# Kernel tuning notes

Measured on AMD Instinct MI355X. Metric: run time of the kernel, lower is better.

## Reference

```python
import jax, jax.numpy as jnp
import numpy as np

V, BS, L, H, D, DF = 32000, 2048, 4, 4, 256, 1024
B, T = 2, 2048
DH = D // H


def setup_inputs() -> dict:
    key = jax.random.key(0)
    ks = iter(jax.random.split(key, 32))
    s = 0.02
    rn = lambda shape: jax.random.normal(next(ks), shape, jnp.float32) * s
    inp = {
        'idx': jax.random.randint(next(ks), (B, T), 0, V),
        'tok_emb': rn((V, D)),
        'pos_emb': rn((BS, D)),
        'Wq': rn((L, D, D)), 'bq': jnp.zeros((L, D)),
        'Wk': rn((L, D, D)), 'bk': jnp.zeros((L, D)),
        'Wv': rn((L, D, D)), 'bv': jnp.zeros((L, D)),
        'Wo': rn((L, D, D)), 'bo': jnp.zeros((L, D)),
        'ln1_g': jnp.ones((L, D)), 'ln1_b': jnp.zeros((L, D)),
        'W1': rn((L, D, DF)), 'b1': jnp.zeros((L, DF)),
        'W2': rn((L, DF, D)), 'b2': jnp.zeros((L, D)),
        'ln2_g': jnp.ones((L, D)), 'ln2_b': jnp.zeros((L, D)),
        'lnf_g': jnp.ones((D,)), 'lnf_b': jnp.zeros((D,)),
        'head_W': rn((D, V)), 'head_b': jnp.zeros((V,)),
    }
    return inp


def _layernorm(x, g, b, eps=1e-5):
    mu = jnp.mean(x, axis=-1, keepdims=True)
    var = jnp.mean(jnp.square(x - mu), axis=-1, keepdims=True)
    return (x - mu) * jax.lax.rsqrt(var + eps) * g + b


def reference(idx, tok_emb, pos_emb, Wq, bq, Wk, bk, Wv, bv, Wo, bo,
              ln1_g, ln1_b, W1, b1, W2, b2, ln2_g, ln2_b,
              lnf_g, lnf_b, head_W, head_b):
    b, t = idx.shape
    x = tok_emb[idx] + pos_emb[:t]  # [B,T,D]
    causal = jnp.tril(jnp.ones((t, t), dtype=bool))  # [T,T]
    scale = 1.0 / np.sqrt(DH)
    neg_inf = jnp.finfo(x.dtype).min
    for l in range(L):
        h = _layernorm(x, ln1_g[l], ln1_b[l])
        q = (h @ Wq[l] + bq[l]).reshape(b, t, H, DH)
        k = (h @ Wk[l] + bk[l]).reshape(b, t, H, DH)
        v = (h @ Wv[l] + bv[l]).reshape(b, t, H, DH)
        att = jnp.einsum('bqhd,bkhd->bhqk', q, k) * scale
        att = jnp.where(causal, att, neg_inf)
        att = jax.nn.softmax(att, axis=-1)
        y = jnp.einsum('bhqk,bkhd->bqhd', att, v).reshape(b, t, D)
        x = x + (y @ Wo[l] + bo[l])
        h = _layernorm(x, ln2_g[l], ln2_b[l])
        x = x + (jax.nn.gelu(h @ W1[l] + b1[l], approximate=False) @ W2[l] + b2[l])
    x = _layernorm(x, lnf_g, lnf_b)
    return x @ head_W + head_b  # [B,T,V]
```

## Files before the change

### kernel.cpp

```cpp
#include <hip/hip_runtime.h>
#include <hip/hip_bf16.h>
#include <math.h>

#define V_   32000
#define L_   4
#define H_   4
#define D_   256
#define DF_  1024
#define B_   2
#define T_   2048
#define DH_  64
#define NTOK (B_*T_)

typedef __attribute__((ext_vector_type(8))) short bf16x8;
typedef __attribute__((ext_vector_type(4))) float f32x4;
typedef unsigned short u16;

#define GLOAD16(gsrc, ldst) \
  __builtin_amdgcn_global_load_lds((const __attribute__((address_space(1))) void*)(gsrc), \
                                   (__attribute__((address_space(3))) void*)(ldst), 16, 0, 0)

#define BAR_A()   asm volatile("s_barrier" ::: "memory")
#define WAITB(N)  do { asm volatile("s_waitcnt vmcnt(" #N ") lgkmcnt(0)" ::: "memory"); \
                       asm volatile("s_barrier" ::: "memory"); } while (0)

__device__ __forceinline__ u16 f2bf(float f) {
    unsigned int u = __builtin_bit_cast(unsigned int, f);
    u = (u + 0x7fff + ((u >> 16) & 1)) >> 16;
    return (u16)u;
}

__device__ __forceinline__ int xcd_swizzle(int orig, int nwg) {
    return ((nwg & 7) == 0) ? ((orig & 7) * (nwg >> 3) + (orig >> 3)) : orig;
}

__global__ __launch_bounds__(256) void prep_kernel(
    const float* __restrict__ Wq, const float* __restrict__ Wk,
    const float* __restrict__ Wv, const float* __restrict__ Wo,
    const float* __restrict__ W1, const float* __restrict__ W2,
    const float* __restrict__ hW,
    u16* __restrict__ WqkvT, u16* __restrict__ WoT,
    u16* __restrict__ W1T, u16* __restrict__ W2T, u16* __restrict__ hWT)
{
    int b = blockIdx.x;
    const float* src; u16* dst; int K, N, k0, n0;
    if (b < 512) {
        int m = b >> 5, t = b & 31;
        int wt = m & 3, l = m >> 2;
        K = 256; N = 256;
        src = (wt == 0 ? Wq : wt == 1 ? Wk : wt == 2 ? Wv : Wo) + (size_t)l * 65536;
        dst = (wt < 3) ? WqkvT + (size_t)l * 196608 + (size_t)wt * 65536
                       : WoT + (size_t)l * 65536;
        k0 = (t >> 3) * 64; n0 = (t & 7) * 32;
    } else if (b < 1024) {
        int bb = b - 512; int l = bb >> 7, t = bb & 127;
        K = 256; N = 1024;
        src = W1 + (size_t)l * 262144; dst = W1T + (size_t)l * 262144;
        k0 = (t >> 5) * 64; n0 = (t & 31) * 32;
    } else if (b < 1536) {
        int bb = b - 1024; int l = bb >> 7, t = bb & 127;
        K = 1024; N = 256;
        src = W2 + (size_t)l * 262144; dst = W2T + (size_t)l * 262144;
        k0 = (t >> 3) * 64; n0 = (t & 7) * 32;
    } else {
        int bb = b - 1536;
        K = 256; N = 32000;
        src = hW; dst = hWT;
        k0 = (bb / 1000) * 64; n0 = (bb % 1000) * 32;
    }
    __shared__ float tile[64][33];
    int tid = threadIdx.x;
    int tc = tid & 31, tr = tid >> 5;
    #pragma unroll
    for (int i = 0; i < 8; i++)
        tile[tr + i*8][tc] = src[(size_t)(k0 + tr + i*8) * N + n0 + tc];
    __syncthreads();
    int kc = tid & 63, nr = tid >> 6;
    #pragma unroll
    for (int i = 0; i < 8; i++)
        dst[(size_t)(n0 + nr + i*4) * K + k0 + kc] = f2bf(tile[kc][nr + i*4]);
}

__global__ __launch_bounds__(256) void embed_qkv_kernel(
    const int* __restrict__ idx, const float* __restrict__ tok, const float* __restrict__ pos,
    const float* __restrict__ g, const float* __restrict__ bta,
    const u16* __restrict__ WqkvT0,
    const float* __restrict__ bq, const float* __restrict__ bk, const float* __restrict__ bv,
    float* __restrict__ x, u16* __restrict__ qkv)
{
    __shared__ u16 Bs[2][256*64];
    __shared__ u16 hS[16][264];

    int tid = threadIdx.x;
    int lane = tid & 63, w = tid >> 6;
    int lr = lane & 15, lg = lane >> 4;
    int bid = xcd_swizzle(blockIdx.x, 256);
    int row0 = bid * 16;

    {
        int grow = tid >> 4;
        int gcol = (tid & 15) * 16;
        int n = row0 + grow;
        int t = n & (T_ - 1);
        int id = idx[n];
        float vv[16];
        #pragma unroll
        for (int i = 0; i < 4; i++) {
            float4 a = *(const float4*)(tok + (size_t)id * D_ + gcol + i * 4);
            float4 b = *(const float4*)(pos + (size_t)t * D_ + gcol + i * 4);
            vv[i*4+0] = a.x + b.x; vv[i*4+1] = a.y + b.y;
            vv[i*4+2] = a.z + b.z; vv[i*4+3] = a.w + b.w;
        }
        float s = 0.f, q = 0.f;
        #pragma unroll
        for (int i = 0; i < 16; i++) { s += vv[i]; q += vv[i]*vv[i]; }
        #pragma unroll
        for (int o = 1; o <= 8; o <<= 1) { s += __shfl_xor(s, o); q += __shfl_xor(q, o); }
        float mu = s * (1.0f / D_);
        float var = q * (1.0f / D_) - mu * mu;
        float ri = rsqrtf(var + 1e-5f);
        #pragma unroll
        for (int i = 0; i < 16; i++) {
            x[(size_t)n * D_ + gcol + i] = vv[i];
            hS[grow][gcol + i] = f2bf((vv[i] - mu) * ri * g[gcol + i] + bta[gcol + i]);
        }
    }

    auto stageQ = [&](int buf, int u) {
        const u16* BT = WqkvT0 + (size_t)(u >> 2) * 65536;
        int k0 = (u & 3) * 64;
        #pragma unroll
        for (int i = 0; i < 8; i++) {
            int o16 = tid + i * 256;
            int r = o16 >> 3;
            int sw = ((o16 & 7) << 4) ^ ((r & 7) << 4);
            GLOAD16(BT + (size_t)r * 256 + k0 + (sw >> 1), &Bs[buf][o16 * 8]);
        }
    };
    auto afH = [&](int t, int ks) -> bf16x8 {
        return *(const bf16x8*)(&hS[lr][(t * 128 + ks * 64 + lg * 16) >> 1]);
    };
    auto bfr = [&](int buf, int ni, int ks) -> bf16x8 {
        int rr = w * 64 + ni * 16 + lr;
        return *(const bf16x8*)(&Bs[buf][rr * 64 + (((ks * 64 + lg * 16) ^ ((rr & 7) << 4)) >> 1)]);
    };

    stageQ(0, 0);
    f32x4 acc[4] = {};
    for (int u = 0; u < 12; u++) {
        BAR_A();
        if (u + 1 < 12) { stageQ((u + 1) & 1, u + 1); WAITB(8); }
        else            { WAITB(0); }
        int t = u & 3;
        #pragma unroll
        for (int ks = 0; ks < 2; ks++) {
            bf16x8 a = afH(t, ks);
            __builtin_amdgcn_s_setprio(1);
            #pragma unroll
            for (int ni = 0; ni < 4; ni++)
                acc[ni] = __builtin_amdgcn_mfma_f32_16x16x32_bf16(a, bfr(u & 1, ni, ks), acc[ni], 0, 0, 0);
            __builtin_amdgcn_s_setprio(0);
        }
        if (t == 3) {
            int sel = u >> 2;
            const float* bp = sel == 0 ? bq : sel == 1 ? bk : bv;
            #pragma unroll
            for (int ni = 0; ni < 4; ni++) {
                #pragma unroll
                for (int j = 0; j < 4; j++) {
                    int row = row0 + lg * 4 + j;
                    int cc = w * 64 + ni * 16 + lr;
                    float v = acc[ni][j] + bp[cc];
                    int bb = row >> 11, tt = row & (T_ - 1);
                    int hh = cc >> 6, dh = cc & 63;
                    qkv[(size_t)sel * NTOK * D_ +
                        ((((size_t)bb * H_ + hh) * T_) + tt) * DH_ + dh] = f2bf(v);
                }
                acc[ni] = (f32x4){0.f, 0.f, 0.f, 0.f};
            }
        }
    }
}

__global__ __launch_bounds__(256) void wo_ln_kernel(
    const u16* __restrict__ ybuf, const u16* __restrict__ WoT, const float* __restrict__ bo,
    const float* __restrict__ ln2g, const float* __restrict__ ln2b,
    float* __restrict__ x, u16* __restrict__ hbuf)
{
    __shared__ u16 As[2][16*64];
    __shared__ u16 Bs[2][256*64];
    __shared__ float sred[4][16], qred[4][16];

    int tid = threadIdx.x;
    int lane = tid & 63, w = tid >> 6;
    int lr = lane & 15, lg = lane >> 4;
    int bid = xcd_swizzle(blockIdx.x, 256);
    int row0 = bid * 16;

    auto stage = [&](int buf, int k0) {
        #pragma unroll
        for (int i = 0; i < 8; i++) {
            int o16 = tid + i * 256;
            int r = o16 >> 3;
            int sw = ((o16 & 7) << 4) ^ ((r & 7) << 4);
            GLOAD16(WoT + (size_t)r * 256 + k0 + (sw >> 1), &Bs[buf][o16 * 8]);
        }
        if (tid < 128) {
            int r = tid >> 3;
            int sw = ((tid & 7) << 4) ^ ((r & 7) << 4);
            GLOAD16(ybuf + (size_t)(row0 + r) * 256 + k0 + (sw >> 1), &As[buf][tid * 8]);
        }
    };
    auto afA = [&](int buf, int ks) -> bf16x8 {
        return *(const bf16x8*)(&As[buf][lr * 64 + (((ks * 64 + lg * 16) ^ ((lr & 7) << 4)) >> 1)]);
    };
    auto bfr = [&](int buf, int ni, int ks) -> bf16x8 {
        int rr = w * 64 + ni * 16 + lr;
        return *(const bf16x8*)(&Bs[buf][rr * 64 + (((ks * 64 + lg * 16) ^ ((rr & 7) << 4)) >> 1)]);
    };

    stage(0, 0);
    f32x4 acc[4] = {};
    for (int t = 0; t < 4; t++) {
        BAR_A();
        if (t + 1 < 4) { stage((t + 1) & 1, (t + 1) * 64); WAITB(8); }
        else           { WAITB(0); }
        #pragma unroll
        for (int ks = 0; ks < 2; ks++) {
            bf16x8 a = afA(t & 1, ks);
            __builtin_amdgcn_s_setprio(1);
            #pragma unroll
            for (int ni = 0; ni < 4; ni++)
                acc[ni] = __builtin_amdgcn_mfma_f32_16x16x32_bf16(a, bfr(t & 1, ni, ks), acc[ni], 0, 0, 0);
            __builtin_amdgcn_s_setprio(0);
        }
    }

    float vals[4][4];
    float rs[4] = {0,0,0,0}, rq[4] = {0,0,0,0};
    #pragma unroll
    for (int ni = 0; ni < 4; ni++)
        #pragma unroll
        for (int j = 0; j < 4; j++) {
            int row = row0 + lg * 4 + j;
            int col = w * 64 + ni * 16 + lr;
            float v = acc[ni][j] + bo[col] + x[(size_t)row * D_ + col];
            x[(size_t)row * D_ + col] = v;
            vals[ni][j] = v;
            rs[j] += v; rq[j] += v * v;
        }
    #pragma unroll
    for (int j = 0; j < 4; j++)
        #pragma unroll
        for (int o = 1; o <= 8; o <<= 1) { rs[j] += __shfl_xor(rs[j], o); rq[j] += __shfl_xor(rq[j], o); }
    if (lr == 0)
        #pragma unroll
        for (int j = 0; j < 4; j++) { sred[w][lg*4 + j] = rs[j]; qred[w][lg*4 + j] = rq[j]; }
    __syncthreads();
    #pragma unroll
    for (int j = 0; j < 4; j++) {
        int r = lg * 4 + j;
        float mu = (sred[0][r] + sred[1][r] + sred[2][r] + sred[3][r]) * (1.0f / D_);
        float var = (qred[0][r] + qred[1][r] + qred[2][r] + qred[3][r]) * (1.0f / D_) - mu * mu;
        float ri = rsqrtf(var + 1e-5f);
        int row = row0 + r;
        #pragma unroll
        for (int ni = 0; ni < 4; ni++) {
            int col = w * 64 + ni * 16 + lr;
            hbuf[(size_t)row * D_ + col] = f2bf((vals[ni][j] - mu) * ri * ln2g[col] + ln2b[col]);
        }
    }
}

__global__ __launch_bounds__(256) void ff1_kernel(
    const u16* __restrict__ A, const u16* __restrict__ BT,
    const float* __restrict__ bias, u16* __restrict__ C)
{
    __shared__ u16 As[2][64*64];
    __shared__ u16 Bs[2][64*64];
    int tid = threadIdx.x;
    int lane = tid & 63, w = tid >> 6;
    int lr = lane & 15, lg = lane >> 4;
    int wm = w >> 1, wn = w & 1;

    int gx = gridDim.x;
    int nwg = gx * gridDim.y;
    int orig = blockIdx.y * gx + blockIdx.x;
    int bid = xcd_swizzle(orig, nwg);
    int row0 = (bid / gx) * 64, col0 = (bid % gx) * 64;

    auto stage = [&](int buf, int k0) {
        #pragma unroll
        for (int i = 0; i < 2; i++) {
            int o16 = tid + i * 256;
            int r = o16 >> 3;
            int sw = ((o16 & 7) << 4) ^ ((r & 7) << 4);
            GLOAD16(A + (size_t)(row0 + r) * 256 + k0 + (sw >> 1), &As[buf][o16 * 8]);
            GLOAD16(BT + (size_t)(col0 + r) * 256 + k0 + (sw >> 1), &Bs[buf][o16 * 8]);
        }
    };

    stage(0, 0);
    f32x4 acc[2][2] = {};
    for (int t = 0; t < 4; t++) {
        BAR_A();
        if (t + 1 < 4) { stage((t + 1) & 1, (t + 1) * 64); WAITB(4); }
        else           { WAITB(0); }
        #pragma unroll
        for (int ks = 0; ks < 2; ks++) {
            bf16x8 af[2], bfv[2];
            #pragma unroll
            for (int mi = 0; mi < 2; mi++) {
                int rr = wm * 32 + mi * 16 + lr;
                af[mi] = *(const bf16x8*)(&As[t & 1][rr * 64 + (((ks * 64 + lg * 16) ^ ((rr & 7) << 4)) >> 1)]);
            }
            #pragma unroll
            for (int ni = 0; ni < 2; ni++) {
                int rr = wn * 32 + ni * 16 + lr;
                bfv[ni] = *(const bf16x8*)(&Bs[t & 1][rr * 64 + (((ks * 64 + lg * 16) ^ ((rr & 7) << 4)) >> 1)]);
            }
            __builtin_amdgcn_s_setprio(1);
            #pragma unroll
            for (int mi = 0; mi < 2; mi++)
                #pragma unroll
                for (int ni = 0; ni < 2; ni++)
                    acc[mi][ni] = __builtin_amdgcn_mfma_f32_16x16x32_bf16(af[mi], bfv[ni], acc[mi][ni], 0, 0, 0);
            __builtin_amdgcn_s_setprio(0);
        }
    }

    #pragma unroll
    for (int mi = 0; mi < 2; mi++)
        #pragma unroll
        for (int ni = 0; ni < 2; ni++)
            #pragma unroll
            for (int j = 0; j < 4; j++) {
                int row = row0 + wm * 32 + mi * 16 + lg * 4 + j;
                int col = col0 + wn * 32 + ni * 16 + lr;
                float v = acc[mi][ni][j] + bias[col];
                v = 0.5f * v * (1.0f + erff(v * 0.70710678118f));
                C[(size_t)row * DF_ + col] = f2bf(v);
            }
}

template<bool LAST>
__global__ __launch_bounds__(256) void ff2qkv_kernel(
    const u16* __restrict__ ff, const u16* __restrict__ W2T, const float* __restrict__ b2,
    const float* __restrict__ lng, const float* __restrict__ lnb,
    const u16* __restrict__ WqkvT,
    const float* __restrict__ bq, const float* __restrict__ bk, const float* __restrict__ bv,
    float* __restrict__ x, u16* __restrict__ hout, u16* __restrict__ qkv)
{
    __shared__ u16 As[2][16*64];
    __shared__ u16 Bs[2][256*64];
    __shared__ u16 hS[16][264];
    __shared__ float sred[4][16], qred[4][16];

    int tid = threadIdx.x;
    int lane = tid & 63, w = tid >> 6;
    int lr = lane & 15, lg = lane >> 4;
    int bid = xcd_swizzle(blockIdx.x, 256);
    int row0 = bid * 16;

    auto stageB = [&](int buf, const u16* BT, int K, int k0) {
        #pragma unroll
        for (int i = 0; i < 8; i++) {
            int o16 = tid + i * 256;
            int r = o16 >> 3;
            int sw = ((o16 & 7) << 4) ^ ((r & 7) << 4);
            GLOAD16(BT + (size_t)r * K + k0 + (sw >> 1), &Bs[buf][o16 * 8]);
        }
    };
    auto stageA = [&](int buf, int k0) {
        if (tid < 128) {
            int r = tid >> 3;
            int sw = ((tid & 7) << 4) ^ ((r & 7) << 4);
            GLOAD16(ff + (size_t)(row0 + r) * DF_ + k0 + (sw >> 1), &As[buf][tid * 8]);
        }
    };
    auto prefetch = [&](int u) {
        if (u < 16) { stageA(u & 1, u * 64); stageB(u & 1, W2T, 1024, u * 64); }
        else if (!LAST && u < 28) {
            int v = u - 16;
            stageB(u & 1, WqkvT + (size_t)(v >> 2) * 65536, 256, (v & 3) * 64);
        }
    };
    auto afA = [&](int buf, int ks) -> bf16x8 {
        return *(const bf16x8*)(&As[buf][lr * 64 + (((ks * 64 + lg * 16) ^ ((lr & 7) << 4)) >> 1)]);
    };
    auto afH = [&](int t, int ks) -> bf16x8 {
        return *(const bf16x8*)(&hS[lr][(t * 128 + ks * 64 + lg * 16) >> 1]);
    };
    auto bfr = [&](int buf, int ni, int ks) -> bf16x8 {
        int rr = w * 64 + ni * 16 + lr;
        return *(const bf16x8*)(&Bs[buf][rr * 64 + (((ks * 64 + lg * 16) ^ ((rr & 7) << 4)) >> 1)]);
    };

    prefetch(0);
    f32x4 acc[4] = {};
    for (int u = 0; u < 16; u++) {
        BAR_A();
        prefetch(u + 1);
        WAITB(8);
        #pragma unroll
        for (int ks = 0; ks < 2; ks++) {
            bf16x8 a = afA(u & 1, ks);
            __builtin_amdgcn_s_setprio(1);
            #pragma unroll
            for (int ni = 0; ni < 4; ni++)
                acc[ni] = __builtin_amdgcn_mfma_f32_16x16x32_bf16(a, bfr(u & 1, ni, ks), acc[ni], 0, 0, 0);
            __builtin_amdgcn_s_setprio(0);
        }
    }

    {
        float vals[4][4];
        float rs[4] = {0,0,0,0}, rq[4] = {0,0,0,0};
        #pragma unroll
        for (int ni = 0; ni < 4; ni++)
            #pragma unroll
            for (int j = 0; j < 4; j++) {
                int row = row0 + lg * 4 + j;
                int col = w * 64 + ni * 16 + lr;
                float v = acc[ni][j] + b2[col] + x[(size_t)row * D_ + col];
                x[(size_t)row * D_ + col] = v;
                vals[ni][j] = v;
                rs[j] += v; rq[j] += v * v;
            }
        #pragma unroll
        for (int j = 0; j < 4; j++)
            #pragma unroll
            for (int o = 1; o <= 8; o <<= 1) { rs[j] += __shfl_xor(rs[j], o); rq[j] += __shfl_xor(rq[j], o); }
        if (lr == 0)
            #pragma unroll
            for (int j = 0; j < 4; j++) { sred[w][lg*4 + j] = rs[j]; qred[w][lg*4 + j] = rq[j]; }
        __syncthreads();
        #pragma unroll
        for (int j = 0; j < 4; j++) {
            int r = lg * 4 + j;
            float mu = (sred[0][r] + sred[1][r] + sred[2][r] + sred[3][r]) * (1.0f / D_);
            float var = (qred[0][r] + qred[1][r] + qred[2][r] + qred[3][r]) * (1.0f / D_) - mu * mu;
            float ri = rsqrtf(var + 1e-5f);
            #pragma unroll
            for (int ni = 0; ni < 4; ni++) {
                int col = w * 64 + ni * 16 + lr;
                float hv = (vals[ni][j] - mu) * ri * lng[col] + lnb[col];
                if (LAST) hout[(size_t)(row0 + r) * D_ + col] = f2bf(hv);
                else      hS[r][col] = f2bf(hv);
            }
        }
    }

    if constexpr (!LAST) {
        __syncthreads();
        f32x4 accT[4] = {};
        for (int v = 0; v < 12; v++) {
            BAR_A();
            if (v + 1 < 12) { prefetch(16 + v + 1); WAITB(8); }
            else            { WAITB(0); }
            int t = v & 3;
            #pragma unroll
            for (int ks = 0; ks < 2; ks++) {
                bf16x8 a = afH(t, ks);
                __builtin_amdgcn_s_setprio(1);
                #pragma unroll
                for (int ni = 0; ni < 4; ni++)
                    accT[ni] = __builtin_amdgcn_mfma_f32_16x16x32_bf16(a, bfr(v & 1, ni, ks), accT[ni], 0, 0, 0);
                __builtin_amdgcn_s_setprio(0);
            }
            if (t == 3) {
                int sel = v >> 2;
                const float* bp = sel == 0 ? bq : sel == 1 ? bk : bv;
                #pragma unroll
                for (int ni = 0; ni < 4; ni++) {
                    #pragma unroll
                    for (int j = 0; j < 4; j++) {
                        int row = row0 + lg * 4 + j;
                        int cc = w * 64 + ni * 16 + lr;
                        float val = accT[ni][j] + bp[cc];
                        int bb = row >> 11, tt = row & (T_ - 1);
                        int hh = cc >> 6, dh = cc & 63;
                        qkv[(size_t)sel * NTOK * D_ +
                            ((((size_t)bb * H_ + hh) * T_) + tt) * DH_ + dh] = f2bf(val);
                    }
                    accT[ni] = (f32x4){0.f, 0.f, 0.f, 0.f};
                }
            }
        }
    }
}

__global__ __launch_bounds__(256) void attn_kernel(
    const u16* __restrict__ q, const u16* __restrict__ k,
    const u16* __restrict__ v, u16* __restrict__ y)
{
    int linear = blockIdx.y * gridDim.x + blockIdx.x;
    int half = linear >> 8, rem = linear & 255;
    int qt_raw = rem & 63;
    int qt = half ? 63 - qt_raw : qt_raw;
    int bh = (rem >> 6) + half * 4;
    int bidx = bh >> 2, h = bh & 3;
    const u16* qp = q + (size_t)bh * T_ * DH_;
    const u16* kp = k + (size_t)bh * T_ * DH_;
    const u16* vp = v + (size_t)bh * T_ * DH_;

    int nch = (qt + 2) >> 1;

    __shared__ u16 Qs[32*64];
    __shared__ u16 Ks[2][2][64*64];
    __shared__ u16 VT[2][64*72];
    __shared__ u16 Ps[4][16*72];

    int tid = threadIdx.x;
    int lane = tid & 63, w = tid >> 6;
    int lr = lane & 15, lg = lane >> 4;
    int p = w >> 1;
    int rh = w & 1;
    int cnt0 = (nch + 1) >> 1, cnt1 = nch >> 1;
    int mycnt = p ? cnt1 : cnt0;
    int maxit = cnt0;

    int pp = tid >> 7;
    int ppcnt = pp ? cnt1 : cnt0;
    int vkey = tid & 63;
    int vdh0 = ((tid >> 6) & 1) * 8;

    {
        int o16 = tid, r = o16 >> 3;
        int sw = ((o16 & 7) << 4) ^ ((r & 7) << 4);
        GLOAD16(qp + (size_t)(qt * 32 + r) * DH_ + (sw >> 1), &Qs[o16 * 8]);
    }
    #pragma unroll
    for (int pr = 0; pr < 2; pr++) {
        int c = min(pr, nch - 1);
        #pragma unroll
        for (int i = 0; i < 2; i++) {
            int o16 = tid + i * 256, r = o16 >> 3;
            int sw = ((o16 & 7) << 4) ^ ((r & 7) << 4);
            GLOAD16(kp + (size_t)(c * 64 + r) * DH_ + (sw >> 1), &Ks[0][pr][o16 * 8]);
        }
    }
    bf16x8 vr[4];
    {
        int c = min(pp, nch - 1);
        #pragma unroll
        for (int g = 0; g < 4; g++)
            vr[g] = *(const bf16x8*)(vp + (size_t)(c * 64 + vkey) * DH_ + vdh0 + g * 16);
    }
    __syncthreads();
    #pragma unroll
    for (int g = 0; g < 4; g++)
        #pragma unroll
        for (int e = 0; e < 8; e++)
            VT[pp][(vdh0 + g * 16 + e) * 72 + vkey] = (u16)vr[g][e];
    bf16x8 qa[2];
    #pragma unroll
    for (int ks = 0; ks < 2; ks++) {
        int rr = rh * 16 + lr;
        qa[ks] = *(const bf16x8*)(Qs + rr * 64 + (((ks * 64 + lg * 16) ^ ((rr & 7) << 4)) >> 1));
    }
    __syncthreads();

    float m[4], lden[4];
    f32x4 o[4] = {};
    #pragma unroll
    for (int j = 0; j < 4; j++) { m[j] = -1e30f; lden[j] = 0.0f; }

    for (int it = 0; it < maxit; it++) {
        int cur = it & 1;
        if (it + 1 < maxit) {
            #pragma unroll
            for (int pr = 0; pr < 2; pr++) {
                int c = min(2 * (it + 1) + pr, nch - 1);
                #pragma unroll
                for (int i = 0; i < 2; i++) {
                    int o16 = tid + i * 256, r = o16 >> 3;
                    int sw = ((o16 & 7) << 4) ^ ((r & 7) << 4);
                    GLOAD16(kp + (size_t)(c * 64 + r) * DH_ + (sw >> 1), &Ks[cur ^ 1][pr][o16 * 8]);
                }
            }
        }
        bool vnext = (it + 1 < ppcnt);
        if (vnext) {
            int c = 2 * (it + 1) + pp;
            #pragma unroll
            for (int g = 0; g < 4; g++)
                vr[g] = *(const bf16x8*)(vp + (size_t)(c * 64 + vkey) * DH_ + vdh0 + g * 16);
        }

        bool act = (it < mycnt);
        if (act) {
            int myc = 2 * it + p;
            f32x4 sc[4];
            #pragma unroll
            for (int ct = 0; ct < 4; ct++) {
                f32x4 s = {};
                __builtin_amdgcn_s_setprio(1);
                #pragma unroll
                for (int ks = 0; ks < 2; ks++) {
                    int rr = ct * 16 + lr;
                    bf16x8 kb = *(const bf16x8*)(&Ks[cur][p][rr * 64 + (((ks * 64 + lg * 16) ^ ((rr & 7) << 4)) >> 1)]);
                    s = __builtin_amdgcn_mfma_f32_16x16x32_bf16(qa[ks], kb, s, 0, 0, 0);
                }
                __builtin_amdgcn_s_setprio(0);
                sc[ct] = s;
            }
            float mloc[4];
            #pragma unroll
            for (int j = 0; j < 4; j++) mloc[j] = -1e30f;
            #pragma unroll
            for (int ct = 0; ct < 4; ct++)
                #pragma unroll
                for (int j = 0; j < 4; j++) {
                    float s = sc[ct][j] * 0.125f;
                    int key = myc * 64 + ct * 16 + lr;
                    int qrow = qt * 32 + rh * 16 + lg * 4 + j;
                    if (key > qrow) s = -1e30f;
                    sc[ct][j] = s;
                    mloc[j] = fmaxf(mloc[j], s);
                }
            #pragma unroll
            for (int j = 0; j < 4; j++) {
                mloc[j] = fmaxf(mloc[j], __shfl_xor(mloc[j], 1));
                mloc[j] = fmaxf(mloc[j], __shfl_xor(mloc[j], 2));
                mloc[j] = fmaxf(mloc[j], __shfl_xor(mloc[j], 4));
                mloc[j] = fmaxf(mloc[j], __shfl_xor(mloc[j], 8));
            }
            float f[4], rs[4];
            #pragma unroll
            for (int j = 0; j < 4; j++) {
                float nm = fmaxf(m[j], mloc[j]);
                f[j] = __expf(m[j] - nm);
                m[j] = nm;
                rs[j] = 0.0f;
            }
            #pragma unroll
            for (int ct = 0; ct < 4; ct++)
                #pragma unroll
                for (int j = 0; j < 4; j++) {
                    float pv = __expf(sc[ct][j] - m[j]);
                    rs[j] += pv;
                    Ps[w][(lg * 4 + j) * 72 + ct * 16 + lr] = f2bf(pv);
                }
            #pragma unroll
            for (int j = 0; j < 4; j++) {
                rs[j] += __shfl_xor(rs[j], 1);
                rs[j] += __shfl_xor(rs[j], 2);
                rs[j] += __shfl_xor(rs[j], 4);
                rs[j] += __shfl_xor(rs[j], 8);
                lden[j] = lden[j] * f[j] + rs[j];
            }
            #pragma unroll
            for (int dt = 0; dt < 4; dt++)
                #pragma unroll
                for (int j = 0; j < 4; j++)
                    o[dt][j] *= f[j];
            #pragma unroll
            for (int ks = 0; ks < 2; ks++) {
                bf16x8 pa = *(const bf16x8*)(&Ps[w][lr * 72 + ks * 32 + lg * 8]);
                __builtin_amdgcn_s_setprio(1);
                #pragma unroll
                for (int dt = 0; dt < 4; dt++) {
                    bf16x8 vb = *(const bf16x8*)(&VT[p][(dt * 16 + lr) * 72 + ks * 32 + lg * 8]);
                    o[dt] = __builtin_amdgcn_mfma_f32_16x16x32_bf16(pa, vb, o[dt], 0, 0, 0);
                }
                __builtin_amdgcn_s_setprio(0);
            }
        }
        __syncthreads();
        if (vnext) {
            #pragma unroll
            for (int g = 0; g < 4; g++)
                #pragma unroll
                for (int e = 0; e < 8; e++)
                    VT[pp][(vdh0 + g * 16 + e) * 72 + vkey] = (u16)vr[g][e];
        }
        __syncthreads();
    }

    float* mg = (float*)&Ks[0][0][0];
    if (p == 1) {
        int base = (rh * 64 + lane) * 24;
        #pragma unroll
        for (int dt = 0; dt < 4; dt++)
            #pragma unroll
            for (int j = 0; j < 4; j++)
                mg[base + dt * 4 + j] = o[dt][j];
        #pragma unroll
        for (int j = 0; j < 4; j++) { mg[base + 16 + j] = m[j]; mg[base + 20 + j] = lden[j]; }
    }
    __syncthreads();
    if (p == 0) {
        int base = (rh * 64 + lane) * 24;
        #pragma unroll
        for (int j = 0; j < 4; j++) {
            float m1 = mg[base + 16 + j];
            float l1 = mg[base + 20 + j];
            float mf = fmaxf(m[j], m1);
            float e0 = __expf(m[j] - mf), e1 = __expf(m1 - mf);
            float inv = 1.0f / (lden[j] * e0 + l1 * e1);
            int qrow = qt * 32 + rh * 16 + lg * 4 + j;
            size_t ybase = ((size_t)(bidx * T_ + qrow)) * D_ + h * DH_;
            #pragma unroll
            for (int dt = 0; dt < 4; dt++) {
                float of = (o[dt][j] * e0 + mg[base + dt * 4 + j] * e1) * inv;
                y[ybase + dt * 16 + lr] = f2bf(of);
            }
        }
    }
}

__global__ __launch_bounds__(256) void head_gemm(
    const u16* __restrict__ A, const u16* __restrict__ BT,
    const float* __restrict__ bias, float* __restrict__ C,
    int M, int N, int K)
{
    __shared__ u16 As[2][128*64];
    __shared__ u16 Bs[2][128*64];
    int tid = threadIdx.x;
    int lane = tid & 63, w = tid >> 6;
    int lr = lane & 15, lg = lane >> 4;
    int wm = w >> 1, wn = w & 1;

    int orig = blockIdx.y * gridDim.x + blockIdx.x;
    int bid = xcd_swizzle(orig, 8000);
    int col0 = (bid >> 5) * 128;
    int row0 = (bid & 31) * 128;

    f32x4 acc[4][4] = {};

    auto stage = [&](int buf, int k0) {
        #pragma unroll
        for (int i = 0; i < 4; i++) {
            int o16 = tid + i * 256;
            int r = o16 >> 3;
            int sw = ((o16 & 7) << 4) ^ ((r & 7) << 4);
            GLOAD16(A + (size_t)(row0 + r) * K + k0 + (sw >> 1), &As[buf][o16 * 8]);
            GLOAD16(BT + (size_t)(col0 + r) * K + k0 + (sw >> 1), &Bs[buf][o16 * 8]);
        }
    };

    stage(0, 0);
    int nk = K >> 6;
    for (int t = 0; t < nk; t++) {
        int cur = t & 1;
        BAR_A();
        if (t + 1 < nk) { stage(cur ^ 1, (t + 1) << 6); WAITB(8); }
        else            { WAITB(0); }
        #pragma unroll
        for (int ks = 0; ks < 2; ks++) {
            bf16x8 af[4], bfr[4];
            #pragma unroll
            for (int mi = 0; mi < 4; mi++) {
                int rr = wm * 64 + mi * 16 + lr;
                af[mi] = *(const bf16x8*)(&As[cur][rr * 64 + (((ks * 64 + lg * 16) ^ ((rr & 7) << 4)) >> 1)]);
            }
            #pragma unroll
            for (int ni = 0; ni < 4; ni++) {
                int rr = wn * 64 + ni * 16 + lr;
                bfr[ni] = *(const bf16x8*)(&Bs[cur][rr * 64 + (((ks * 64 + lg * 16) ^ ((rr & 7) << 4)) >> 1)]);
            }
            __builtin_amdgcn_s_setprio(1);
            #pragma unroll
            for (int mi = 0; mi < 4; mi++)
                #pragma unroll
                for (int ni = 0; ni < 4; ni++)
                    acc[mi][ni] = __builtin_amdgcn_mfma_f32_16x16x32_bf16(af[mi], bfr[ni], acc[mi][ni], 0, 0, 0);
            __builtin_amdgcn_s_setprio(0);
        }
    }

    #pragma unroll
    for (int mi = 0; mi < 4; mi++)
        #pragma unroll
        for (int ni = 0; ni < 4; ni++)
            #pragma unroll
            for (int j = 0; j < 4; j++) {
                int row = row0 + wm * 64 + mi * 16 + lg * 4 + j;
                int col = col0 + wn * 64 + ni * 16 + lr;
                __builtin_nontemporal_store(acc[mi][ni][j] + bias[col], &C[(size_t)row * N + col]);
            }
}

extern "C" void kernel_launch(void* const* d_in, const int* in_sizes, int n_in,
                              void* d_out, int out_size, void* d_ws, size_t ws_size,
                              hipStream_t stream)
{
    const int*   idx  = (const int*)d_in[0];
    const float* tok  = (const float*)d_in[1];
    const float* pos  = (const float*)d_in[2];
    const float* Wq   = (const float*)d_in[3];
    const float* bq   = (const float*)d_in[4];
    const float* Wk   = (const float*)d_in[5];
    const float* bk   = (const float*)d_in[6];
    const float* Wv   = (const float*)d_in[7];
    const float* bv   = (const float*)d_in[8];
    const float* Wo   = (const float*)d_in[9];
    const float* bo   = (const float*)d_in[10];
    const float* ln1g = (const float*)d_in[11];
    const float* ln1b = (const float*)d_in[12];
    const float* W1   = (const float*)d_in[13];
    const float* b1   = (const float*)d_in[14];
    const float* W2   = (const float*)d_in[15];
    const float* b2   = (const float*)d_in[16];
    const float* ln2g = (const float*)d_in[17];
    const float* ln2b = (const float*)d_in[18];
    const float* lnfg = (const float*)d_in[19];
    const float* lnfb = (const float*)d_in[20];
    const float* hW   = (const float*)d_in[21];
    const float* hb   = (const float*)d_in[22];

    char* p = (char*)d_ws;
    float* x     = (float*)p;           p += (size_t)NTOK * D_ * 4;
    u16* hbuf    = (u16*)p;             p += (size_t)NTOK * D_ * 2;
    u16* qkvbuf  = (u16*)p;             p += (size_t)3 * NTOK * D_ * 2;
    u16* ybuf    = (u16*)p;             p += (size_t)NTOK * D_ * 2;
    u16* ff      = (u16*)p;             p += (size_t)NTOK * DF_ * 2;
    u16* WqkvT   = (u16*)p;             p += (size_t)L_ * 768 * D_ * 2;
    u16* WoT     = (u16*)p;             p += (size_t)L_ * D_ * D_ * 2;
    u16* W1T     = (u16*)p;             p += (size_t)L_ * D_ * DF_ * 2;
    u16* W2T     = (u16*)p;             p += (size_t)L_ * DF_ * D_ * 2;
    u16* hWT     = (u16*)p;             p += (size_t)V_ * D_ * 2;

    u16* qbuf = qkvbuf;
    u16* kbuf = qkvbuf + (size_t)NTOK * D_;
    u16* vbuf = qkvbuf + (size_t)2 * NTOK * D_;

    prep_kernel<<<5536, 256, 0, stream>>>(Wq, Wk, Wv, Wo, W1, W2, hW,
                                          WqkvT, WoT, W1T, W2T, hWT);

    embed_qkv_kernel<<<256, 256, 0, stream>>>(idx, tok, pos, ln1g, ln1b,
                                              WqkvT, bq, bk, bv, x, qkvbuf);

    dim3 gAttn(64, 8);
    dim3 gFF1(DF_ / 64, NTOK / 64);
    for (int l = 0; l < L_; l++) {
        attn_kernel<<<gAttn, 256, 0, stream>>>(qbuf, kbuf, vbuf, ybuf);
        wo_ln_kernel<<<256, 256, 0, stream>>>(ybuf, WoT + (size_t)l * 65536, bo + l * D_,
                                              ln2g + l * D_, ln2b + l * D_, x, hbuf);
        ff1_kernel<<<gFF1, 256, 0, stream>>>(hbuf, W1T + (size_t)l * 262144, b1 + l * DF_, ff);
        if (l < L_ - 1) {
            ff2qkv_kernel<false><<<256, 256, 0, stream>>>(
                ff, W2T + (size_t)l * 262144, b2 + l * D_,
                ln1g + (l + 1) * D_, ln1b + (l + 1) * D_,
                WqkvT + (size_t)(l + 1) * 196608,
                bq + (l + 1) * D_, bk + (l + 1) * D_, bv + (l + 1) * D_,
                x, nullptr, qkvbuf);
        } else {
            ff2qkv_kernel<true><<<256, 256, 0, stream>>>(
                ff, W2T + (size_t)l * 262144, b2 + l * D_,
                lnfg, lnfb,
                nullptr, nullptr, nullptr, nullptr,
                x, hbuf, nullptr);
        }
    }

    dim3 gHead(V_ / 128, NTOK / 128);
    head_gemm<<<gHead, 256, 0, stream>>>(hbuf, hWT, hb, (float*)d_out, NTOK, V_, D_);
}
```

Before: 501.3 us.

## Prefetch residual early, triple-buffer FF1 K loop, stage head output through LDS

New measurement: 479.0 us. 4.4% less time.

```diff
diff --git a/kernel.cpp b/kernel.cpp
--- a/kernel.cpp
+++ b/kernel.cpp
@@ -197,6 +197,13 @@
     int bid = xcd_swizzle(blockIdx.x, 256);
     int row0 = bid * 16;
 
+    float xv[4][4];
+    #pragma unroll
+    for (int ni = 0; ni < 4; ni++)
+        #pragma unroll
+        for (int j = 0; j < 4; j++)
+            xv[ni][j] = x[(size_t)(row0 + lg * 4 + j) * D_ + w * 64 + ni * 16 + lr];
+
     auto stage = [&](int buf, int k0) {
         #pragma unroll
         for (int i = 0; i < 8; i++) {
@@ -244,7 +251,7 @@
         for (int j = 0; j < 4; j++) {
             int row = row0 + lg * 4 + j;
             int col = w * 64 + ni * 16 + lr;
-            float v = acc[ni][j] + bo[col] + x[(size_t)row * D_ + col];
+            float v = acc[ni][j] + bo[col] + xv[ni][j];
             x[(size_t)row * D_ + col] = v;
             vals[ni][j] = v;
             rs[j] += v; rq[j] += v * v;
@@ -276,8 +283,8 @@
     const u16* __restrict__ A, const u16* __restrict__ BT,
     const float* __restrict__ bias, u16* __restrict__ C)
 {
-    __shared__ u16 As[2][64*64];
-    __shared__ u16 Bs[2][64*64];
+    __shared__ u16 As[3][64*64];
+    __shared__ u16 Bs[3][64*64];
     int tid = threadIdx.x;
     int lane = tid & 63, w = tid >> 6;
     int lr = lane & 15, lg = lane >> 4;
@@ -300,24 +307,20 @@
         }
     };
 
-    stage(0, 0);
     f32x4 acc[2][2] = {};
-    for (int t = 0; t < 4; t++) {
-        BAR_A();
-        if (t + 1 < 4) { stage((t + 1) & 1, (t + 1) * 64); WAITB(4); }
-        else           { WAITB(0); }
+    auto compute = [&](int buf) {
         #pragma unroll
         for (int ks = 0; ks < 2; ks++) {
             bf16x8 af[2], bfv[2];
             #pragma unroll
             for (int mi = 0; mi < 2; mi++) {
                 int rr = wm * 32 + mi * 16 + lr;
-                af[mi] = *(const bf16x8*)(&As[t & 1][rr * 64 + (((ks * 64 + lg * 16) ^ ((rr & 7) << 4)) >> 1)]);
+                af[mi] = *(const bf16x8*)(&As[buf][rr * 64 + (((ks * 64 + lg * 16) ^ ((rr & 7) << 4)) >> 1)]);
             }
             #pragma unroll
             for (int ni = 0; ni < 2; ni++) {
                 int rr = wn * 32 + ni * 16 + lr;
-                bfv[ni] = *(const bf16x8*)(&Bs[t & 1][rr * 64 + (((ks * 64 + lg * 16) ^ ((rr & 7) << 4)) >> 1)]);
+                bfv[ni] = *(const bf16x8*)(&Bs[buf][rr * 64 + (((ks * 64 + lg * 16) ^ ((rr & 7) << 4)) >> 1)]);
             }
             __builtin_amdgcn_s_setprio(1);
             #pragma unroll
@@ -327,7 +330,23 @@
                     acc[mi][ni] = __builtin_amdgcn_mfma_f32_16x16x32_bf16(af[mi], bfv[ni], acc[mi][ni], 0, 0, 0);
             __builtin_amdgcn_s_setprio(0);
         }
-    }
+    };
+
+    stage(0, 0); stage(1, 64);
+    asm volatile("s_waitcnt vmcnt(4) lgkmcnt(0)" ::: "memory");
+    asm volatile("s_barrier" ::: "memory");
+    stage(2, 128);
+    compute(0);
+    asm volatile("s_waitcnt vmcnt(4) lgkmcnt(0)" ::: "memory");
+    asm volatile("s_barrier" ::: "memory");
+    stage(0, 192);
+    compute(1);
+    asm volatile("s_waitcnt vmcnt(4) lgkmcnt(0)" ::: "memory");
+    asm volatile("s_barrier" ::: "memory");
+    compute(2);
+    asm volatile("s_waitcnt vmcnt(0) lgkmcnt(0)" ::: "memory");
+    asm volatile("s_barrier" ::: "memory");
+    compute(0);
 
     #pragma unroll
     for (int mi = 0; mi < 2; mi++)
@@ -362,6 +381,13 @@
     int bid = xcd_swizzle(blockIdx.x, 256);
     int row0 = bid * 16;
 
+    float xv[4][4];
+    #pragma unroll
+    for (int ni = 0; ni < 4; ni++)
+        #pragma unroll
+        for (int j = 0; j < 4; j++)
+            xv[ni][j] = x[(size_t)(row0 + lg * 4 + j) * D_ + w * 64 + ni * 16 + lr];
+
     auto stageB = [&](int buf, const u16* BT, int K, int k0) {
         #pragma unroll
         for (int i = 0; i < 8; i++) {
@@ -422,7 +448,7 @@
             for (int j = 0; j < 4; j++) {
                 int row = row0 + lg * 4 + j;
                 int col = w * 64 + ni * 16 + lr;
-                float v = acc[ni][j] + b2[col] + x[(size_t)row * D_ + col];
+                float v = acc[ni][j] + b2[col] + xv[ni][j];
                 x[(size_t)row * D_ + col] = v;
                 vals[ni][j] = v;
                 rs[j] += v; rq[j] += v * v;
@@ -715,8 +741,9 @@
     const float* __restrict__ bias, float* __restrict__ C,
     int M, int N, int K)
 {
-    __shared__ u16 As[2][128*64];
-    __shared__ u16 Bs[2][128*64];
+    __shared__ u16 smem[32768];
+    u16* As = smem;
+    u16* Bs = smem + 16384;
     int tid = threadIdx.x;
     int lane = tid & 63, w = tid >> 6;
     int lr = lane & 15, lg = lane >> 4;
@@ -735,8 +762,8 @@
             int o16 = tid + i * 256;
             int r = o16 >> 3;
             int sw = ((o16 & 7) << 4) ^ ((r & 7) << 4);
-            GLOAD16(A + (size_t)(row0 + r) * K + k0 + (sw >> 1), &As[buf][o16 * 8]);
-            GLOAD16(BT + (size_t)(col0 + r) * K + k0 + (sw >> 1), &Bs[buf][o16 * 8]);
+            GLOAD16(A + (size_t)(row0 + r) * K + k0 + (sw >> 1), &As[buf * 8192 + o16 * 8]);
+            GLOAD16(BT + (size_t)(col0 + r) * K + k0 + (sw >> 1), &Bs[buf * 8192 + o16 * 8]);
         }
     };
 
@@ -753,12 +780,12 @@
             #pragma unroll
             for (int mi = 0; mi < 4; mi++) {
                 int rr = wm * 64 + mi * 16 + lr;
-                af[mi] = *(const bf16x8*)(&As[cur][rr * 64 + (((ks * 64 + lg * 16) ^ ((rr & 7) << 4)) >> 1)]);
+                af[mi] = *(const bf16x8*)(&As[cur * 8192 + rr * 64 + (((ks * 64 + lg * 16) ^ ((rr & 7) << 4)) >> 1)]);
             }
             #pragma unroll
             for (int ni = 0; ni < 4; ni++) {
                 int rr = wn * 64 + ni * 16 + lr;
-                bfr[ni] = *(const bf16x8*)(&Bs[cur][rr * 64 + (((ks * 64 + lg * 16) ^ ((rr & 7) << 4)) >> 1)]);
+                bfr[ni] = *(const bf16x8*)(&Bs[cur * 8192 + rr * 64 + (((ks * 64 + lg * 16) ^ ((rr & 7) << 4)) >> 1)]);
             }
             __builtin_amdgcn_s_setprio(1);
             #pragma unroll
@@ -770,16 +797,28 @@
         }
     }
 
+    float* tS = (float*)smem;
+    __syncthreads();
     #pragma unroll
     for (int mi = 0; mi < 4; mi++)
         #pragma unroll
         for (int ni = 0; ni < 4; ni++)
             #pragma unroll
             for (int j = 0; j < 4; j++) {
-                int row = row0 + wm * 64 + mi * 16 + lg * 4 + j;
-                int col = col0 + wn * 64 + ni * 16 + lr;
-                __builtin_nontemporal_store(acc[mi][ni][j] + bias[col], &C[(size_t)row * N + col]);
-            }
+                int rl = wm * 64 + mi * 16 + lg * 4 + j;
+                int cl = wn * 64 + ni * 16 + lr;
+                int ch = (cl >> 2) ^ (rl & 7);
+                tS[rl * 128 + ch * 4 + (cl & 3)] = acc[mi][ni][j] + bias[col0 + cl];
+            }
+    __syncthreads();
+    int cc = tid & 31, r0l = (tid >> 5) * 16;
+    #pragma unroll
+    for (int i = 0; i < 16; i++) {
+        int rl = r0l + i;
+        int sch = cc ^ (rl & 7);
+        f32x4 v4 = *(const f32x4*)&tS[rl * 128 + sch * 4];
+        __builtin_nontemporal_store(v4, (f32x4*)&C[(size_t)(row0 + rl) * N + col0 + cc * 4]);
+    }
 }
 
 extern "C" void kernel_launch(void* const* d_in, const int* in_sizes, int n_in,
```
